# Performance work log

Measured on AMD Instinct MI355X. Metric: run time of the kernel, lower is better.

The kernel has to match this reference:

```python
import jax, jax.numpy as jnp
import numpy as np

G, NP, C, H, L = 64, 512, 128, 4, 4
N = G * NP            # 32768 nodes
E = N * 16            # 524288 edges
HD = C // H
BN_EPS = 1e-5


def _bn(x, g, b):
    # BatchNorm1d, training-mode (biased batch statistics over nodes)
    m = x.mean(axis=0)
    v = jnp.var(x, axis=0)
    return (x - m) * jax.lax.rsqrt(v + BN_EPS) * g + b


def setup_inputs() -> dict:
    key = jax.random.key(0)
    ks = iter(jax.random.split(key, 64))
    rn = lambda shape, s=0.05: jax.random.normal(next(ks), shape, jnp.float32) * s
    inp = {}
    inp["x"] = jax.random.normal(next(ks), (N, 32), jnp.float32)
    inp["edge_attr"] = jax.random.normal(next(ks), (E, 16), jnp.float32)
    epg = E // G  # edges per graph; endpoints stay within each graph
    off = jnp.repeat(jnp.arange(G), epg) * NP
    src = jax.random.randint(next(ks), (E,), 0, NP) + off
    dst = jax.random.randint(next(ks), (E,), 0, NP) + off
    inp["edge_index"] = jnp.stack([src, dst]).astype(jnp.int32)
    inp["batch"] = jnp.repeat(jnp.arange(G), NP).astype(jnp.int32)
    inp["np_w"] = rn((32, C)); inp["np_b"] = jnp.zeros((C,), jnp.float32)
    inp["ep_w"] = rn((16, C)); inp["ep_b"] = jnp.zeros((C,), jnp.float32)
    inp["eps"] = jnp.zeros((L,), jnp.float32)  # GINEConv train_eps, init 0
    inp["gine_w1"] = rn((L, C, 2 * C)); inp["gine_b1"] = jnp.zeros((L, 2 * C), jnp.float32)
    inp["gine_w2"] = rn((L, 2 * C, C)); inp["gine_b2"] = jnp.zeros((L, C), jnp.float32)
    inp["attn_in_w"] = rn((L, 3 * C, C)); inp["attn_in_b"] = jnp.zeros((L, 3 * C), jnp.float32)
    inp["attn_out_w"] = rn((L, C, C)); inp["attn_out_b"] = jnp.zeros((L, C), jnp.float32)
    ones = jnp.ones((L, C), jnp.float32); zeros = jnp.zeros((L, C), jnp.float32)
    inp["bn1_g"], inp["bn1_b"] = ones, zeros
    inp["bn2_g"], inp["bn2_b"] = ones, zeros
    inp["bn3_g"], inp["bn3_b"] = ones, zeros
    inp["mlp_w1"] = rn((L, C, 2 * C)); inp["mlp_b1"] = jnp.zeros((L, 2 * C), jnp.float32)
    inp["mlp_w2"] = rn((L, 2 * C, C)); inp["mlp_b2"] = jnp.zeros((L, C), jnp.float32)
    inp["ln_g"] = jnp.ones((2 * C,), jnp.float32); inp["ln_b"] = jnp.zeros((2 * C,), jnp.float32)
    inp["head_w1"] = rn((2 * C, C)); inp["head_b1"] = jnp.zeros((C,), jnp.float32)
    inp["head_w2"] = rn((C, 1)); inp["head_b2"] = jnp.zeros((1,), jnp.float32)
    return inp


def reference(x, edge_attr, np_w, np_b, ep_w, ep_b, eps,
              gine_w1, gine_b1, gine_w2, gine_b2,
              attn_in_w, attn_in_b, attn_out_w, attn_out_b,
              bn1_g, bn1_b, bn2_g, bn2_b, bn3_g, bn3_b,
              mlp_w1, mlp_b1, mlp_w2, mlp_b2,
              ln_g, ln_b, head_w1, head_b1, head_w2, head_b2,
              edge_index, batch):
    h = x @ np_w + np_b                       # [N, C]
    e = edge_attr @ ep_w + ep_b               # [E, C]
    src, dst = edge_index[0], edge_index[1]   # PyG: row=source j, col=target i
    scale = 1.0 / np.sqrt(HD).astype(np.float32)
    for l in range(L):
        # ---- local GINEConv: relu(x_j + e) scatter-sum -> GELU MLP ----
        msg = jax.nn.relu(h[src] + e)                                 # [E, C]
        aggr = jax.ops.segment_sum(msg, dst, num_segments=N)          # [N, C]
        z = (1.0 + eps[l]) * h + aggr
        z = jax.nn.gelu(z @ gine_w1[l] + gine_b1[l], approximate=False) @ gine_w2[l] + gine_b2[l]
        h_local = _bn(z + h, bn1_g[l], bn1_b[l])
        # ---- global multihead attention on dense per-graph batch ----
        xd = h.reshape(G, NP, C)
        qkv = xd @ attn_in_w[l].T + attn_in_b[l]                      # [G, NP, 3C]
        q, k, v = jnp.split(qkv, 3, axis=-1)
        split_heads = lambda t: t.reshape(G, NP, H, HD).transpose(0, 2, 1, 3)
        q, k, v = split_heads(q), split_heads(k), split_heads(v)
        att = jax.nn.softmax(jnp.einsum('ghqd,ghkd->ghqk', q, k) * scale, axis=-1)
        o = jnp.einsum('ghqk,ghkd->ghqd', att, v).transpose(0, 2, 1, 3).reshape(N, C)
        o = o @ attn_out_w[l].T + attn_out_b[l]
        h_attn = _bn(o + h, bn2_g[l], bn2_b[l])
        # ---- combine + FFN ----
        out = h_local + h_attn
        m = jax.nn.relu(out @ mlp_w1[l] + mlp_b1[l]) @ mlp_w2[l] + mlp_b2[l]
        h = _bn(out + m, bn3_g[l], bn3_b[l])
    # ---- mean || max pooling over graphs ----
    cnt = jax.ops.segment_sum(jnp.ones((N, 1), h.dtype), batch, num_segments=G)
    x_mean = jax.ops.segment_sum(h, batch, num_segments=G) / cnt
    x_max = jax.ops.segment_max(h, batch, num_segments=G)
    g = jnp.concatenate([x_mean, x_max], axis=-1)                     # [G, 2C]
    mu = g.mean(-1, keepdims=True)
    var = jnp.var(g, axis=-1, keepdims=True)
    g = (g - mu) * jax.lax.rsqrt(var + 1e-5) * ln_g + ln_b
    g = jax.nn.gelu(g @ head_w1 + head_b1, approximate=False) @ head_w2 + head_b2
    return g.squeeze(-1)                                              # [G]
```

## Files before the change

kernel.cpp:

```cpp
#include <hip/hip_runtime.h>
#include <math.h>

typedef _Float16 f16;
typedef _Float16 f16x2 __attribute__((ext_vector_type(2)));
typedef _Float16 f16x4 __attribute__((ext_vector_type(4)));
typedef _Float16 f16x8 __attribute__((ext_vector_type(8)));
typedef float f32x4 __attribute__((ext_vector_type(4)));

#define G_ 64
#define NP_ 512
#define N_ 32768
#define E_ 524288
#define C_ 128
#define H_ 4
#define HD_ 32
#define L_ 4

static __device__ __forceinline__ float gelu_exact(float x) {
    return 0.5f * x * (1.0f + erff(x * 0.70710678118654752f));
}

__global__ __launch_bounds__(256) void k_prep(
    const float* __restrict__ g1, const float* __restrict__ g2,
    const float* __restrict__ m1, const float* __restrict__ m2,
    const float* __restrict__ ai, const float* __restrict__ ao,
    f16* __restrict__ g1t, f16* __restrict__ g2t,
    f16* __restrict__ m1t, f16* __restrict__ m2t,
    f16* __restrict__ ait, f16* __restrict__ aot)
{
    int i = blockIdx.x * 256 + threadIdx.x;
    if (i < 131072) {
        int l = i >> 15, r = i & 32767;
        int k = r >> 8, m = r & 255;
        g1t[l * 32768 + m * 128 + k] = (f16)g1[i];
    } else if (i < 262144) {
        int j = i - 131072;
        int l = j >> 15, r = j & 32767;
        int k = r >> 7, m = r & 127;
        g2t[l * 32768 + m * 256 + k] = (f16)g2[j];
    } else if (i < 393216) {
        int j = i - 262144;
        int l = j >> 15, r = j & 32767;
        int k = r >> 8, m = r & 255;
        m1t[l * 32768 + m * 128 + k] = (f16)m1[j];
    } else if (i < 524288) {
        int j = i - 393216;
        int l = j >> 15, r = j & 32767;
        int k = r >> 7, m = r & 127;
        m2t[l * 32768 + m * 256 + k] = (f16)m2[j];
    } else if (i < 720896) {
        int j = i - 524288;
        ait[j] = (f16)ai[j];
    } else if (i < 786432) {
        int j = i - 720896;
        aot[j] = (f16)ao[j];
    }
}

__global__ __launch_bounds__(256) void k_h0(const float* __restrict__ x,
    const float* __restrict__ w, const float* __restrict__ b,
    f16* __restrict__ h16)
{
    const int tid = threadIdx.x;
    const int lane = tid & 63, wid = tid >> 6;
    const int node = blockIdx.x * 4 + wid;
    const int c2 = lane * 2;
    float a0 = b[c2], a1 = b[c2 + 1];
    const float* xr = x + (size_t)node * 32;
#pragma unroll
    for (int k = 0; k < 32; k++) {
        float xv = xr[k];
        a0 += xv * w[k * 128 + c2];
        a1 += xv * w[k * 128 + c2 + 1];
    }
    f16x2 z; z[0] = (f16)a0; z[1] = (f16)a1;
    *(f16x2*)(h16 + (size_t)node * 128 + c2) = z;
}

__global__ void k_zero2(int* a, int* b) {
    int i = blockIdx.x * 256 + threadIdx.x;
    a[i] = 0; b[i] = 0;
}
__global__ void k_count(const int* __restrict__ ei, int* __restrict__ counts) {
    int e = blockIdx.x * 256 + threadIdx.x;
    atomicAdd(&counts[ei[E_ + e]], 1);
}
__global__ __launch_bounds__(1024) void k_scan(const int* __restrict__ counts,
                                               int* __restrict__ rowp)
{
    __shared__ int part[1024];
    const int t = threadIdx.x;
    int s = 0;
#pragma unroll
    for (int i = 0; i < 32; i++) s += counts[t * 32 + i];
    part[t] = s;
    __syncthreads();
    for (int off = 1; off < 1024; off <<= 1) {
        int u = (t >= off) ? part[t - off] : 0;
        __syncthreads();
        part[t] += u;
        __syncthreads();
    }
    int run = part[t] - s;
    for (int i = 0; i < 32; i++) {
        int c = counts[t * 32 + i];
        rowp[t * 32 + i] = run;
        run += c;
    }
    if (t == 1023) rowp[N_] = part[1023];
}
__global__ void k_fill(const int* __restrict__ ei, const int* __restrict__ rowp,
                       int* __restrict__ cursor, int* __restrict__ srcp,
                       int* __restrict__ eidp)
{
    int e = blockIdx.x * 256 + threadIdx.x;
    int d = ei[E_ + e];
    int p = atomicAdd(&cursor[d], 1);
    int pos = rowp[d] + p;
    srcp[pos] = ei[e];
    eidp[pos] = e;
}

__global__ __launch_bounds__(256) void k_edge(const float* __restrict__ edge_attr,
    const float* __restrict__ epw, const float* __restrict__ epb,
    const int* __restrict__ eidp, f16* __restrict__ e16p)
{
    __shared__ __align__(16) float rows[4][64][16];
    const int tid = threadIdx.x;
    const int lane = tid & 63, wid = tid >> 6;
    const int c2 = lane * 2;
    float w0[16], w1[16];
#pragma unroll
    for (int k = 0; k < 16; k++) {
        w0[k] = epw[k * 128 + c2];
        w1[k] = epw[k * 128 + c2 + 1];
    }
    const float b0 = epb[c2], b1 = epb[c2 + 1];
    const int gidx = blockIdx.x & 63, chunk = blockIdx.x >> 6;
    const int base = (gidx * 32 + chunk) * 256 + wid * 64;
    const int eidv = eidp[base + lane];
    const int er = lane >> 2, ec = lane & 3;
#pragma unroll
    for (int u = 0; u < 4; u++) {
        int e = __shfl(eidv, u * 16 + er);
        float4 v = *(const float4*)(edge_attr + (size_t)e * 16 + ec * 4);
        *(float4*)(&rows[wid][u * 16 + er][ec * 4]) = v;
    }
    for (int i = 0; i < 64; i++) {
        const float* r = &rows[wid][i][0];
        float4 q0 = *(const float4*)(r);
        float4 q1 = *(const float4*)(r + 4);
        float4 q2 = *(const float4*)(r + 8);
        float4 q3 = *(const float4*)(r + 12);
        float e0 = b0, e1 = b1;
        e0 += q0.x*w0[0] + q0.y*w0[1] + q0.z*w0[2] + q0.w*w0[3]
            + q1.x*w0[4] + q1.y*w0[5] + q1.z*w0[6] + q1.w*w0[7]
            + q2.x*w0[8] + q2.y*w0[9] + q2.z*w0[10] + q2.w*w0[11]
            + q3.x*w0[12] + q3.y*w0[13] + q3.z*w0[14] + q3.w*w0[15];
        e1 += q0.x*w1[0] + q0.y*w1[1] + q0.z*w1[2] + q0.w*w1[3]
            + q1.x*w1[4] + q1.y*w1[5] + q1.z*w1[6] + q1.w*w1[7]
            + q2.x*w1[8] + q2.y*w1[9] + q2.z*w1[10] + q2.w*w1[11]
            + q3.x*w1[12] + q3.y*w1[13] + q3.z*w1[14] + q3.w*w1[15];
        f16x2 z; z[0] = (f16)e0; z[1] = (f16)e1;
        *(f16x2*)(e16p + (size_t)(base + i) * 128 + c2) = z;
    }
}

__global__ __launch_bounds__(256) void k_aggr(const f16* __restrict__ h16,
    const f16* __restrict__ e16p, const int* __restrict__ srcp,
    const int* __restrict__ rowp, const float* __restrict__ eps, int layer,
    f16* __restrict__ zin)
{
    const int tid = threadIdx.x;
    const int lane = tid & 63, wid = tid >> 6;
    const int node = (blockIdx.x & 63) * 512 + (blockIdx.x >> 6) * 4 + wid;
    const int c2 = lane * 2;
    const int r0 = rowp[node], r1 = rowp[node + 1];
    const int deg = r1 - r0;
    const f16x2 hn = *(const f16x2*)(h16 + (size_t)node * 128 + c2);
    float a0 = 0.f, a1 = 0.f;
    if (deg > 0) {
        const int dd = deg < 64 ? deg : 64;
        const int jm = dd - 1;
        const int srcv = srcp[r0 + (lane < jm ? lane : jm)];
        f16x2 h_c, e_c, h_n, e_n;
        {
            int s = __shfl(srcv, 0);
            h_c = *(const f16x2*)(h16 + (size_t)s * 128 + c2);
            e_c = *(const f16x2*)(e16p + (size_t)r0 * 128 + c2);
            int j1 = 1 < jm ? 1 : jm;
            int s1 = __shfl(srcv, j1);
            h_n = *(const f16x2*)(h16 + (size_t)s1 * 128 + c2);
            e_n = *(const f16x2*)(e16p + (size_t)(r0 + j1) * 128 + c2);
        }
        for (int j = 0; j < dd; ++j) {
            int j2 = j + 2 < jm ? j + 2 : jm;
            int s2 = __shfl(srcv, j2);
            f16x2 h_f = *(const f16x2*)(h16 + (size_t)s2 * 128 + c2);
            f16x2 e_f = *(const f16x2*)(e16p + (size_t)(r0 + j2) * 128 + c2);
            a0 += fmaxf((float)e_c[0] + (float)h_c[0], 0.0f);
            a1 += fmaxf((float)e_c[1] + (float)h_c[1], 0.0f);
            h_c = h_n; e_c = e_n; h_n = h_f; e_n = e_f;
        }
        for (int pos = r0 + 64; pos < r1; ++pos) {
            int s = srcp[pos];
            f16x2 ev = *(const f16x2*)(e16p + (size_t)pos * 128 + c2);
            f16x2 hv = *(const f16x2*)(h16 + (size_t)s * 128 + c2);
            a0 += fmaxf((float)ev[0] + (float)hv[0], 0.0f);
            a1 += fmaxf((float)ev[1] + (float)hv[1], 0.0f);
        }
    }
    const float ep = 1.0f + eps[layer];
    f16x2 z;
    z[0] = (f16)(ep * (float)hn[0] + a0);
    z[1] = (f16)(ep * (float)hn[1] + a1);
    *(f16x2*)(zin + (size_t)node * 128 + c2) = z;
}

template <int KD, int EPI, bool COMB>
__global__ __launch_bounds__(256) void k_gemm(
    const f16* __restrict__ A, const f16* __restrict__ Bt,
    const float* __restrict__ bias,
    const f16* __restrict__ r1, const f16* __restrict__ r2,
    const float* __restrict__ sc1, const float* __restrict__ sc2,
    f16* __restrict__ out, f16* __restrict__ aout,
    float* __restrict__ stats, int Mout)
{
    __shared__ __align__(16) f16 As[64 * 40];
    __shared__ __align__(16) f16 Bs[128 * 40];
    __shared__ float sca[4][128];
    __shared__ float sscr[4][2][64];
    const int tid = threadIdx.x;
    const int lane = tid & 63, wid = tid >> 6;
    const int quad = lane >> 4, l16 = lane & 15;
    const int wm = wid >> 1, wn = wid & 1;
    const int rb = blockIdx.x, cb = blockIdx.y;
    if constexpr (COMB) {
        if (tid < 128) { sca[0][tid] = sc1[tid]; sca[1][tid] = sc1[128 + tid]; }
        else { int c = tid - 128; sca[2][c] = sc2[c]; sca[3][c] = sc2[128 + c]; }
    }
    f32x4 acc[2][4];
#pragma unroll
    for (int i = 0; i < 2; i++)
#pragma unroll
        for (int j = 0; j < 4; j++) acc[i][j] = {0.f, 0.f, 0.f, 0.f};
    const int arow0 = rb * 64, brow0 = cb * 128;
    const int srow = tid >> 2, sc4 = tid & 3;
#pragma unroll
    for (int kc = 0; kc < KD / 32; ++kc) {
        __syncthreads();
        if constexpr (COMB) {
            size_t off = (size_t)(arow0 + srow) * KD + kc * 32 + sc4 * 8;
            f16x8 x1 = *(const f16x8*)(r1 + off);
            f16x8 x2 = *(const f16x8*)(r2 + off);
            const int k0 = kc * 32 + sc4 * 8;
            f16x8 zc;
#pragma unroll
            for (int i = 0; i < 8; i++) {
                int k = k0 + i;
                float v = (float)x1[i] * sca[0][k] + sca[1][k]
                        + (float)x2[i] * sca[2][k] + sca[3][k];
                zc[i] = (f16)v;
            }
            *(f16x8*)(As + srow * 40 + sc4 * 8) = zc;
            if (cb == 0) *(f16x8*)(aout + off) = zc;
        } else {
            *(uint4*)(As + srow * 40 + sc4 * 8) =
                *(const uint4*)(A + (size_t)(arow0 + srow) * KD + kc * 32 + sc4 * 8);
        }
#pragma unroll
        for (int i = 0; i < 2; i++) {
            int j = tid + i * 256;
            int br = j >> 2, bc = j & 3;
            *(uint4*)(Bs + br * 40 + bc * 8) =
                *(const uint4*)(Bt + (size_t)(brow0 + br) * KD + kc * 32 + bc * 8);
        }
        __syncthreads();
        f16x8 af[2], bf[4];
#pragma unroll
        for (int mt = 0; mt < 2; mt++)
            af[mt] = *(const f16x8*)(As + (wm * 32 + mt * 16 + l16) * 40 + quad * 8);
#pragma unroll
        for (int nt = 0; nt < 4; nt++)
            bf[nt] = *(const f16x8*)(Bs + (wn * 64 + nt * 16 + l16) * 40 + quad * 8);
#pragma unroll
        for (int mt = 0; mt < 2; mt++)
#pragma unroll
            for (int nt = 0; nt < 4; nt++)
                acc[mt][nt] = __builtin_amdgcn_mfma_f32_16x16x32_f16(
                    af[mt], bf[nt], acc[mt][nt], 0, 0, 0);
    }
    float ssum[4] = {0, 0, 0, 0}, ssq[4] = {0, 0, 0, 0};
#pragma unroll
    for (int nt = 0; nt < 4; nt++) {
        const int col = cb * 128 + wn * 64 + nt * 16 + l16;
        const float bv = bias[col];
#pragma unroll
        for (int mt = 0; mt < 2; mt++) {
#pragma unroll
            for (int r = 0; r < 4; r++) {
                const int row = rb * 64 + wm * 32 + mt * 16 + quad * 4 + r;
                float v = acc[mt][nt][r] + bv;
                if constexpr (EPI == 0) v = gelu_exact(v);
                if constexpr (EPI == 1) v = fmaxf(v, 0.0f);
                if constexpr (EPI == 2) {
                    v += (float)r1[(size_t)row * 128 + col];
                    ssum[nt] += v;
                    ssq[nt] += v * v;
                }
                out[(size_t)row * Mout + col] = (f16)v;
            }
        }
    }
    if constexpr (EPI == 2) {
#pragma unroll
        for (int nt = 0; nt < 4; nt++) {
            float s = ssum[nt], q = ssq[nt];
            s += __shfl_xor(s, 16); s += __shfl_xor(s, 32);
            q += __shfl_xor(q, 16); q += __shfl_xor(q, 32);
            if (lane < 16) {
                sscr[wid][0][nt * 16 + lane] = s;
                sscr[wid][1][nt * 16 + lane] = q;
            }
        }
        __syncthreads();
        if (tid < 128) {
            int c = tid, wnc = c >> 6, jj = c & 63;
            stats[(size_t)rb * 256 + c] = sscr[wnc][0][jj] + sscr[wnc + 2][0][jj];
            stats[(size_t)rb * 256 + 128 + c] = sscr[wnc][1][jj] + sscr[wnc + 2][1][jj];
        }
    }
}

__global__ __launch_bounds__(256) void k_qkv(
    const f16* __restrict__ A, const f16* __restrict__ Bt,
    const float* __restrict__ bias,
    f16* __restrict__ qb, f16* __restrict__ kb, f16* __restrict__ vt)
{
    __shared__ __align__(16) f16 As[64 * 40];
    __shared__ __align__(16) f16 Bs[128 * 40];
    const int tid = threadIdx.x;
    const int lane = tid & 63, wid = tid >> 6;
    const int quad = lane >> 4, l16 = lane & 15;
    const int wm = wid >> 1, wn = wid & 1;
    const int rb = blockIdx.x, cb = blockIdx.y;
    f32x4 acc[2][4];
#pragma unroll
    for (int i = 0; i < 2; i++)
#pragma unroll
        for (int j = 0; j < 4; j++) acc[i][j] = {0.f, 0.f, 0.f, 0.f};
    const int arow0 = rb * 64, brow0 = cb * 128;
    const int srow = tid >> 2, sc4 = tid & 3;
#pragma unroll
    for (int kc = 0; kc < 4; ++kc) {
        __syncthreads();
        *(uint4*)(As + srow * 40 + sc4 * 8) =
            *(const uint4*)(A + (size_t)(arow0 + srow) * 128 + kc * 32 + sc4 * 8);
#pragma unroll
        for (int i = 0; i < 2; i++) {
            int j = tid + i * 256;
            int br = j >> 2, bc = j & 3;
            *(uint4*)(Bs + br * 40 + bc * 8) =
                *(const uint4*)(Bt + (size_t)(brow0 + br) * 128 + kc * 32 + bc * 8);
        }
        __syncthreads();
        f16x8 af[2], bf[4];
#pragma unroll
        for (int mt = 0; mt < 2; mt++)
            af[mt] = *(const f16x8*)(As + (wm * 32 + mt * 16 + l16) * 40 + quad * 8);
#pragma unroll
        for (int nt = 0; nt < 4; nt++)
            bf[nt] = *(const f16x8*)(Bs + (wn * 64 + nt * 16 + l16) * 40 + quad * 8);
#pragma unroll
        for (int mt = 0; mt < 2; mt++)
#pragma unroll
            for (int nt = 0; nt < 4; nt++)
                acc[mt][nt] = __builtin_amdgcn_mfma_f32_16x16x32_f16(
                    af[mt], bf[nt], acc[mt][nt], 0, 0, 0);
    }
    if (cb < 2) {
        f16* outp = cb ? kb : qb;
#pragma unroll
        for (int nt = 0; nt < 4; nt++) {
            const int col = wn * 64 + nt * 16 + l16;
            const float bv = bias[cb * 128 + col];
#pragma unroll
            for (int mt = 0; mt < 2; mt++) {
#pragma unroll
                for (int r = 0; r < 4; r++) {
                    const int row = rb * 64 + wm * 32 + mt * 16 + quad * 4 + r;
                    outp[(size_t)row * 128 + col] = (f16)(acc[mt][nt][r] + bv);
                }
            }
        }
    } else {
        const int g = rb >> 3;
#pragma unroll
        for (int nt = 0; nt < 4; nt++) {
            const int coll = wn * 64 + nt * 16 + l16;
            const int h = coll >> 5, d = coll & 31;
            const float bv = bias[256 + coll];
#pragma unroll
            for (int mt = 0; mt < 2; mt++) {
                const int n0 = (rb & 7) * 64 + wm * 32 + mt * 16 + quad * 4;
                f16x4 z;
#pragma unroll
                for (int r = 0; r < 4; r++) z[r] = (f16)(acc[mt][nt][r] + bv);
                *(f16x4*)(vt + ((size_t)((g * 4 + h) * 32 + d)) * 512 + n0) = z;
            }
        }
    }
}

__global__ __launch_bounds__(1024) void k_fin(
    const float* __restrict__ sA, const float* __restrict__ sB,
    const float* __restrict__ g1, const float* __restrict__ b1,
    const float* __restrict__ g2, const float* __restrict__ b2,
    float* __restrict__ o1, float* __restrict__ o2)
{
    __shared__ float rS[8][128], rQ[8][128];
    const float* s = blockIdx.x ? sB : sA;
    const float* g = blockIdx.x ? g2 : g1;
    const float* bb = blockIdx.x ? b2 : b1;
    float* o = blockIdx.x ? o2 : o1;
    const int c = threadIdx.x & 127, seg = threadIdx.x >> 7;
    float S = 0, Q = 0;
    for (int b = seg * 64; b < seg * 64 + 64; b++) {
        S += s[b * 256 + c];
        Q += s[b * 256 + 128 + c];
    }
    rS[seg][c] = S; rQ[seg][c] = Q;
    __syncthreads();
    if (threadIdx.x < 128) {
        float Ss = 0, Qs = 0;
#pragma unroll
        for (int k = 0; k < 8; k++) { Ss += rS[k][c]; Qs += rQ[k][c]; }
        float mean = Ss * (1.0f / 32768.0f);
        float var = Qs * (1.0f / 32768.0f) - mean * mean;
        float rstd = rsqrtf(var + 1e-5f);
        float scv = g[c] * rstd;
        o[c] = scv;
        o[128 + c] = bb[c] - mean * scv;
    }
}

__global__ __launch_bounds__(256) void k_bn3(const f16* __restrict__ t3,
    const float* __restrict__ s3, f16* __restrict__ h16)
{
    int i = blockIdx.x * 256 + threadIdx.x;
    int n = i >> 6, c2 = (i & 63) * 2;
    f16x2 a = *(const f16x2*)(t3 + (size_t)n * 128 + c2);
    f16x2 z;
    z[0] = (f16)((float)a[0] * s3[c2] + s3[128 + c2]);
    z[1] = (f16)((float)a[1] * s3[c2 + 1] + s3[129 + c2]);
    *(f16x2*)(h16 + (size_t)n * 128 + c2) = z;
}

__global__ __launch_bounds__(256) void k_attn(const f16* __restrict__ qb,
    const f16* __restrict__ kb, const f16* __restrict__ vt, f16* __restrict__ o)
{
    __shared__ __align__(16) f16 Ks[512 * 36];
    __shared__ __align__(16) f16 Ps[4][512];
    const int tid = threadIdx.x;
    const int lane = tid & 63, wid = tid >> 6;
    const int quad = lane >> 4, l16 = lane & 15;
    const int blk = blockIdx.x;
    const int gh = blk & 255, qc = blk >> 8;
    const int g = gh >> 2, h = gh & 3;
#pragma unroll
    for (int i = 0; i < 8; i++) {
        int j = i * 256 + tid;
        int n = j >> 2, c4 = j & 3;
        *(uint4*)(Ks + n * 36 + c4 * 8) =
            *(const uint4*)(kb + (size_t)(g * 512 + n) * 128 + h * 32 + c4 * 8);
    }
    const int node = g * 512 + qc * 64 + wid * 16 + l16;
    f16x8 aq = *(const f16x8*)(qb + (size_t)node * 128 + h * 32 + quad * 8);
    __syncthreads();
    const f32x4 zero = {0.f, 0.f, 0.f, 0.f};
    const float cexp = 0.17677669529663689f * 1.44269504088896341f;
    float m = -1e30f;
    for (int kt = 0; kt < 32; ++kt) {
        f16x8 ak = *(const f16x8*)(Ks + (kt * 16 + l16) * 36 + quad * 8);
        f32x4 s = __builtin_amdgcn_mfma_f32_16x16x32_f16(ak, aq, zero, 0, 0, 0);
        m = fmaxf(m, fmaxf(fmaxf(s[0], s[1]), fmaxf(s[2], s[3])));
    }
    m = fmaxf(m, __shfl_xor(m, 16));
    m = fmaxf(m, __shfl_xor(m, 32));
    float lsum = 0.f;
    f32x4 o0 = {0.f, 0.f, 0.f, 0.f}, o1 = {0.f, 0.f, 0.f, 0.f};
    f16* pp = &Ps[wid][0];
    const f16* vbase = vt + (size_t)gh * 32 * 512;
    const int roff = quad * 128;
    for (int ch = 0; ch < 16; ++ch) {
        f16x8 ak0 = *(const f16x8*)(Ks + ((2 * ch) * 16 + l16) * 36 + quad * 8);
        f16x8 ak1 = *(const f16x8*)(Ks + ((2 * ch + 1) * 16 + l16) * 36 + quad * 8);
        f32x4 s0 = __builtin_amdgcn_mfma_f32_16x16x32_f16(ak0, aq, zero, 0, 0, 0);
        f32x4 s1 = __builtin_amdgcn_mfma_f32_16x16x32_f16(ak1, aq, zero, 0, 0, 0);
        f16x4 p0, p1;
#pragma unroll
        for (int r = 0; r < 4; r++) {
            float e0 = exp2f((s0[r] - m) * cexp);
            float e1 = exp2f((s1[r] - m) * cexp);
            lsum += e0 + e1;
            p0[r] = (f16)e0; p1[r] = (f16)e1;
        }
        *(f16x4*)(pp + lane * 4) = p0;
        *(f16x4*)(pp + 256 + lane * 4) = p1;
        f16x4 a_lo = *(const f16x4*)(pp + roff + l16 * 4);
        f16x4 a_hi = *(const f16x4*)(pp + roff + 64 + l16 * 4);
        f16x8 ap;
#pragma unroll
        for (int i2 = 0; i2 < 4; i2++) { ap[i2] = a_lo[i2]; ap[i2 + 4] = a_hi[i2]; }
        f16x8 bv0 = *(const f16x8*)(vbase + (size_t)l16 * 512 + ch * 32 + quad * 8);
        f16x8 bv1 = *(const f16x8*)(vbase + (size_t)(16 + l16) * 512 + ch * 32 + quad * 8);
        o0 = __builtin_amdgcn_mfma_f32_16x16x32_f16(ap, bv0, o0, 0, 0, 0);
        o1 = __builtin_amdgcn_mfma_f32_16x16x32_f16(ap, bv1, o1, 0, 0, 0);
    }
    lsum += __shfl_xor(lsum, 16);
    lsum += __shfl_xor(lsum, 32);
    const float linv = 1.0f / lsum;
#pragma unroll
    for (int r = 0; r < 4; r++) {
        float li = __shfl(linv, quad * 4 + r);
        int nrow = g * 512 + qc * 64 + wid * 16 + quad * 4 + r;
        o[(size_t)nrow * 128 + h * 32 + l16] = (f16)(o0[r] * li);
        o[(size_t)nrow * 128 + h * 32 + 16 + l16] = (f16)(o1[r] * li);
    }
}

__global__ __launch_bounds__(256) void k_pool(const f16* __restrict__ h16,
    const float* __restrict__ ln_g, const float* __restrict__ ln_b,
    const float* __restrict__ w1, const float* __restrict__ b1,
    const float* __restrict__ w2, const float* __restrict__ b2,
    float* __restrict__ outp)
{
    __shared__ float ssum[4][128], smax[4][128];
    __shared__ float gl[256];
    __shared__ float red[256];
    __shared__ float hid[128];
    __shared__ float stat[2];
    const int tid = threadIdx.x, lane = tid & 63, wid = tid >> 6;
    const int g = blockIdx.x;
    const int c2 = lane * 2;
    float s0 = 0, s1 = 0, m0 = -1e30f, m1 = -1e30f;
    for (int i = 0; i < 128; i++) {
        int n = g * 512 + i * 4 + wid;
        f16x2 hv = *(const f16x2*)(h16 + (size_t)n * 128 + c2);
        float v0 = (float)hv[0], v1 = (float)hv[1];
        s0 += v0; s1 += v1;
        m0 = fmaxf(m0, v0); m1 = fmaxf(m1, v1);
    }
    ssum[wid][c2] = s0; ssum[wid][c2 + 1] = s1;
    smax[wid][c2] = m0; smax[wid][c2 + 1] = m1;
    __syncthreads();
    if (tid < 128) {
        float S = ssum[0][tid] + ssum[1][tid] + ssum[2][tid] + ssum[3][tid];
        float M = fmaxf(fmaxf(smax[0][tid], smax[1][tid]),
                        fmaxf(smax[2][tid], smax[3][tid]));
        gl[tid] = S * (1.0f / 512.0f);
        gl[128 + tid] = M;
    }
    __syncthreads();
    float v = gl[tid];
    red[tid] = v;
    __syncthreads();
    for (int off = 128; off > 0; off >>= 1) {
        if (tid < off) red[tid] += red[tid + off];
        __syncthreads();
    }
    if (tid == 0) stat[0] = red[0] * (1.0f / 256.0f);
    __syncthreads();
    float mu = stat[0];
    red[tid] = (v - mu) * (v - mu);
    __syncthreads();
    for (int off = 128; off > 0; off >>= 1) {
        if (tid < off) red[tid] += red[tid + off];
        __syncthreads();
    }
    if (tid == 0) stat[1] = rsqrtf(red[0] * (1.0f / 256.0f) + 1e-5f);
    __syncthreads();
    float gn = (v - mu) * stat[1] * ln_g[tid] + ln_b[tid];
    __syncthreads();
    gl[tid] = gn;
    __syncthreads();
    if (tid < 128) {
        float a = b1[tid];
        for (int k = 0; k < 256; k++) a += gl[k] * w1[k * 128 + tid];
        hid[tid] = gelu_exact(a);
    }
    __syncthreads();
    if (tid < 64) {
        float a = hid[tid] * w2[tid] + hid[tid + 64] * w2[tid + 64];
        a += __shfl_xor(a, 32); a += __shfl_xor(a, 16); a += __shfl_xor(a, 8);
        a += __shfl_xor(a, 4); a += __shfl_xor(a, 2); a += __shfl_xor(a, 1);
        if (tid == 0) outp[g] = a + b2[0];
    }
}

extern "C" void kernel_launch(void* const* d_in, const int* in_sizes, int n_in,
                              void* d_out, int out_size, void* d_ws, size_t ws_size,
                              hipStream_t stream)
{
    const float* x          = (const float*)d_in[0];
    const float* edge_attr  = (const float*)d_in[1];
    const int*   ei         = (const int*)d_in[2];
    const float* np_w       = (const float*)d_in[4];
    const float* np_b       = (const float*)d_in[5];
    const float* ep_w       = (const float*)d_in[6];
    const float* ep_b       = (const float*)d_in[7];
    const float* eps        = (const float*)d_in[8];
    const float* gine_w1    = (const float*)d_in[9];
    const float* gine_b1    = (const float*)d_in[10];
    const float* gine_w2    = (const float*)d_in[11];
    const float* gine_b2    = (const float*)d_in[12];
    const float* attn_in_w  = (const float*)d_in[13];
    const float* attn_in_b  = (const float*)d_in[14];
    const float* attn_out_w = (const float*)d_in[15];
    const float* attn_out_b = (const float*)d_in[16];
    const float* bn1_g      = (const float*)d_in[17];
    const float* bn1_b      = (const float*)d_in[18];
    const float* bn2_g      = (const float*)d_in[19];
    const float* bn2_b      = (const float*)d_in[20];
    const float* bn3_g      = (const float*)d_in[21];
    const float* bn3_b      = (const float*)d_in[22];
    const float* mlp_w1     = (const float*)d_in[23];
    const float* mlp_b1     = (const float*)d_in[24];
    const float* mlp_w2     = (const float*)d_in[25];
    const float* mlp_b2     = (const float*)d_in[26];
    const float* ln_g       = (const float*)d_in[27];
    const float* ln_b       = (const float*)d_in[28];
    const float* head_w1    = (const float*)d_in[29];
    const float* head_b1    = (const float*)d_in[30];
    const float* head_w2    = (const float*)d_in[31];
    const float* head_b2    = (const float*)d_in[32];

    char* ws = (char*)d_ws;
    size_t off = 0;
    auto alloc = [&](size_t bytes) {
        void* p = ws + off;
        off += (bytes + 255) & ~(size_t)255;
        return p;
    };
    f16*  h16    = (f16*)alloc((size_t)N_ * 128 * 2);
    f16*  zin    = (f16*)alloc((size_t)N_ * 128 * 2);
    f16*  tloc   = (f16*)alloc((size_t)N_ * 128 * 2);
    f16*  tattn  = (f16*)alloc((size_t)N_ * 128 * 2);
    f16*  out16  = (f16*)alloc((size_t)N_ * 128 * 2);
    f16*  o16    = (f16*)alloc((size_t)N_ * 128 * 2);
    f16*  u16    = (f16*)alloc((size_t)N_ * 256 * 2);
    float* statsA = (float*)alloc(512 * 256 * 4);
    float* statsB = (float*)alloc(512 * 256 * 4);
    float* scsh1  = (float*)alloc(256 * 4);
    float* scsh2  = (float*)alloc(256 * 4);
    float* scsh3  = (float*)alloc(256 * 4);
    int*  rowp   = (int*)alloc((N_ + 1) * 4);
    int*  counts = (int*)alloc(N_ * 4);
    int*  cursor = (int*)alloc(N_ * 4);
    int*  srcp   = (int*)alloc((size_t)E_ * 4);
    int*  eidp   = (int*)alloc((size_t)E_ * 4);
    f16*  g1t    = (f16*)alloc((size_t)L_ * 32768 * 2);
    f16*  g2t    = (f16*)alloc((size_t)L_ * 32768 * 2);
    f16*  m1t    = (f16*)alloc((size_t)L_ * 32768 * 2);
    f16*  m2t    = (f16*)alloc((size_t)L_ * 32768 * 2);
    f16*  ait    = (f16*)alloc((size_t)L_ * 49152 * 2);
    f16*  aot    = (f16*)alloc((size_t)L_ * 16384 * 2);
    f16*  e16p   = (f16*)alloc((size_t)E_ * 128 * 2);
    f16*  qbuf = zin;
    f16*  kbuf = out16;
    f16*  vt   = u16 + (size_t)N_ * 128;

    dim3 B(256);
    k_prep<<<dim3(3072), B, 0, stream>>>(gine_w1, gine_w2, mlp_w1, mlp_w2,
                                         attn_in_w, attn_out_w,
                                         g1t, g2t, m1t, m2t, ait, aot);
    k_h0<<<dim3(8192), B, 0, stream>>>(x, np_w, np_b, h16);
    k_zero2<<<dim3(128), B, 0, stream>>>(counts, cursor);
    k_count<<<dim3(2048), B, 0, stream>>>(ei, counts);
    k_scan<<<dim3(1), dim3(1024), 0, stream>>>(counts, rowp);
    k_fill<<<dim3(2048), B, 0, stream>>>(ei, rowp, cursor, srcp, eidp);
    k_edge<<<dim3(2048), B, 0, stream>>>(edge_attr, ep_w, ep_b, eidp, e16p);

    const f16* nf = (const f16*)nullptr;
    const float* nff = (const float*)nullptr;
    for (int l = 0; l < L_; l++) {
        k_aggr<<<dim3(8192), B, 0, stream>>>(h16, e16p, srcp, rowp, eps, l, zin);
        k_gemm<128, 0, false><<<dim3(512, 2), B, 0, stream>>>(
            zin, g1t + l * 32768, gine_b1 + l * 256, nf, nf, nff, nff,
            u16, (f16*)nullptr, (float*)nullptr, 256);
        k_gemm<256, 2, false><<<dim3(512, 1), B, 0, stream>>>(
            u16, g2t + l * 32768, gine_b2 + l * 128, h16, nf, nff, nff,
            tloc, (f16*)nullptr, statsA, 128);
        k_qkv<<<dim3(512, 3), B, 0, stream>>>(
            h16, ait + l * 49152, attn_in_b + l * 384, qbuf, kbuf, vt);
        k_attn<<<dim3(2048), B, 0, stream>>>(qbuf, kbuf, vt, o16);
        k_gemm<128, 2, false><<<dim3(512, 1), B, 0, stream>>>(
            o16, aot + l * 16384, attn_out_b + l * 128, h16, nf, nff, nff,
            tattn, (f16*)nullptr, statsB, 128);
        k_fin<<<dim3(2), dim3(1024), 0, stream>>>(
            statsA, statsB, bn1_g + l * 128, bn1_b + l * 128,
            bn2_g + l * 128, bn2_b + l * 128, scsh1, scsh2);
        k_gemm<128, 1, true><<<dim3(512, 2), B, 0, stream>>>(
            nf, m1t + l * 32768, mlp_b1 + l * 256, tloc, tattn, scsh1, scsh2,
            u16, out16, (float*)nullptr, 256);
        k_gemm<256, 2, false><<<dim3(512, 1), B, 0, stream>>>(
            u16, m2t + l * 32768, mlp_b2 + l * 128, out16, nf, nff, nff,
            zin, (f16*)nullptr, statsA, 128);
        k_fin<<<dim3(1), dim3(1024), 0, stream>>>(
            statsA, statsA, bn3_g + l * 128, bn3_b + l * 128,
            bn3_g + l * 128, bn3_b + l * 128, scsh3, scsh3);
        k_bn3<<<dim3(8192), B, 0, stream>>>(zin, scsh3, h16);
    }
    k_pool<<<dim3(64), B, 0, stream>>>(h16, ln_g, ln_b, head_w1, head_b1,
                                       head_w2, head_b2, (float*)d_out);
}
```

Before: 978.8 us.

## Load GEMM tiles via global_load_lds with XOR swizzle and merge output GEMMs

GEMM kernels now stage the full 128-wide K slab into LDS with direct global-to-LDS loads, using an XOR-swizzled layout instead of padded rows. This removes the per-32-K-chunk barriers and register round trips. The GINE second GEMM and the attention output projection are merged into one launch, k_g2, which splits work by blockIdx.y. The v-transpose buffer is moved to tloc to avoid aliasing u16. In exchange the kernels use more LDS per block, which may lower occupancy, and k_g2 now has a runtime K loop.

```diff
diff --git a/kernel.cpp b/kernel.cpp
--- a/kernel.cpp
+++ b/kernel.cpp
@@ -18,6 +18,12 @@
 
 static __device__ __forceinline__ float gelu_exact(float x) {
     return 0.5f * x * (1.0f + erff(x * 0.70710678118654752f));
+}
+
+static __device__ __forceinline__ void gload_lds(const f16* g, f16* l) {
+    __builtin_amdgcn_global_load_lds(
+        (const __attribute__((address_space(1))) void*)g,
+        (__attribute__((address_space(3))) void*)l, 16, 0, 0);
 }
 
 __global__ __launch_bounds__(256) void k_prep(
@@ -217,72 +223,84 @@
     *(f16x2*)(zin + (size_t)node * 128 + c2) = z;
 }
 
-template <int KD, int EPI, bool COMB>
-__global__ __launch_bounds__(256) void k_gemm(
+
+template <int EPI, bool COMB>
+__global__ __launch_bounds__(256) void k_g128(
     const f16* __restrict__ A, const f16* __restrict__ Bt,
     const float* __restrict__ bias,
     const f16* __restrict__ r1, const f16* __restrict__ r2,
     const float* __restrict__ sc1, const float* __restrict__ sc2,
-    f16* __restrict__ out, f16* __restrict__ aout,
-    float* __restrict__ stats, int Mout)
-{
-    __shared__ __align__(16) f16 As[64 * 40];
-    __shared__ __align__(16) f16 Bs[128 * 40];
+    f16* __restrict__ out, f16* __restrict__ aout, int Mout)
+{
+    __shared__ __align__(16) f16 Sm[3072 * 8];
     __shared__ float sca[4][128];
-    __shared__ float sscr[4][2][64];
+    f16* As = Sm;
+    f16* Bs = Sm + 1024 * 8;
     const int tid = threadIdx.x;
     const int lane = tid & 63, wid = tid >> 6;
     const int quad = lane >> 4, l16 = lane & 15;
     const int wm = wid >> 1, wn = wid & 1;
     const int rb = blockIdx.x, cb = blockIdx.y;
-    if constexpr (COMB) {
+    const int arow0 = rb * 64, brow0 = cb * 128;
+#pragma unroll
+    for (int i = 0; i < 8; i++) {
+        int s = i * 256 + wid * 64 + lane;
+        int r = s >> 4, cg = (s & 15) ^ (r & 7);
+        gload_lds(Bt + (size_t)(brow0 + r) * 128 + cg * 8,
+                  Bs + (size_t)(i * 256 + wid * 64) * 8);
+    }
+    if constexpr (!COMB) {
+#pragma unroll
+        for (int i = 0; i < 4; i++) {
+            int s = i * 256 + wid * 64 + lane;
+            int r = s >> 4, cg = (s & 15) ^ (r & 7);
+            gload_lds(A + (size_t)(arow0 + r) * 128 + cg * 8,
+                      As + (size_t)(i * 256 + wid * 64) * 8);
+        }
+        __syncthreads();
+    } else {
         if (tid < 128) { sca[0][tid] = sc1[tid]; sca[1][tid] = sc1[128 + tid]; }
         else { int c = tid - 128; sca[2][c] = sc2[c]; sca[3][c] = sc2[128 + c]; }
-    }
-    f32x4 acc[2][4];
-#pragma unroll
-    for (int i = 0; i < 2; i++)
-#pragma unroll
-        for (int j = 0; j < 4; j++) acc[i][j] = {0.f, 0.f, 0.f, 0.f};
-    const int arow0 = rb * 64, brow0 = cb * 128;
-    const int srow = tid >> 2, sc4 = tid & 3;
-#pragma unroll
-    for (int kc = 0; kc < KD / 32; ++kc) {
         __syncthreads();
-        if constexpr (COMB) {
-            size_t off = (size_t)(arow0 + srow) * KD + kc * 32 + sc4 * 8;
+#pragma unroll
+        for (int j = 0; j < 4; j++) {
+            int s = j * 256 + tid;
+            int r = s >> 4, cg = (s & 15) ^ (r & 7);
+            size_t off = (size_t)(arow0 + r) * 128 + cg * 8;
             f16x8 x1 = *(const f16x8*)(r1 + off);
             f16x8 x2 = *(const f16x8*)(r2 + off);
-            const int k0 = kc * 32 + sc4 * 8;
             f16x8 zc;
 #pragma unroll
-            for (int i = 0; i < 8; i++) {
-                int k = k0 + i;
-                float v = (float)x1[i] * sca[0][k] + sca[1][k]
-                        + (float)x2[i] * sca[2][k] + sca[3][k];
-                zc[i] = (f16)v;
+            for (int i2 = 0; i2 < 8; i2++) {
+                int k = cg * 8 + i2;
+                float v = (float)x1[i2] * sca[0][k] + sca[1][k]
+                        + (float)x2[i2] * sca[2][k] + sca[3][k];
+                zc[i2] = (f16)v;
             }
-            *(f16x8*)(As + srow * 40 + sc4 * 8) = zc;
+            *(f16x8*)(As + (size_t)s * 8) = zc;
             if (cb == 0) *(f16x8*)(aout + off) = zc;
-        } else {
-            *(uint4*)(As + srow * 40 + sc4 * 8) =
-                *(const uint4*)(A + (size_t)(arow0 + srow) * KD + kc * 32 + sc4 * 8);
-        }
-#pragma unroll
-        for (int i = 0; i < 2; i++) {
-            int j = tid + i * 256;
-            int br = j >> 2, bc = j & 3;
-            *(uint4*)(Bs + br * 40 + bc * 8) =
-                *(const uint4*)(Bt + (size_t)(brow0 + br) * KD + kc * 32 + bc * 8);
         }
         __syncthreads();
+    }
+    f32x4 acc[2][4];
+#pragma unroll
+    for (int i = 0; i < 2; i++)
+#pragma unroll
+        for (int j = 0; j < 4; j++) acc[i][j] = {0.f, 0.f, 0.f, 0.f};
+    const int ra0 = wm * 32 + l16, rb0 = wn * 64 + l16;
+#pragma unroll
+    for (int kc = 0; kc < 4; ++kc) {
         f16x8 af[2], bf[4];
 #pragma unroll
-        for (int mt = 0; mt < 2; mt++)
-            af[mt] = *(const f16x8*)(As + (wm * 32 + mt * 16 + l16) * 40 + quad * 8);
-#pragma unroll
-        for (int nt = 0; nt < 4; nt++)
-            bf[nt] = *(const f16x8*)(Bs + (wn * 64 + nt * 16 + l16) * 40 + quad * 8);
+        for (int mt = 0; mt < 2; mt++) {
+            int r = ra0 + mt * 16;
+            af[mt] = *(const f16x8*)(As + (size_t)(r * 16 + ((kc * 4 + quad) ^ (r & 7))) * 8);
+        }
+#pragma unroll
+        for (int nt = 0; nt < 4; nt++) {
+            int r = rb0 + nt * 16;
+            bf[nt] = *(const f16x8*)(Bs + (size_t)(r * 16 + ((kc * 4 + quad) ^ (r & 7))) * 8);
+        }
 #pragma unroll
         for (int mt = 0; mt < 2; mt++)
 #pragma unroll
@@ -290,7 +308,6 @@
                 acc[mt][nt] = __builtin_amdgcn_mfma_f32_16x16x32_f16(
                     af[mt], bf[nt], acc[mt][nt], 0, 0, 0);
     }
-    float ssum[4] = {0, 0, 0, 0}, ssq[4] = {0, 0, 0, 0};
 #pragma unroll
     for (int nt = 0; nt < 4; nt++) {
         const int col = cb * 128 + wn * 64 + nt * 16 + l16;
@@ -303,74 +320,166 @@
                 float v = acc[mt][nt][r] + bv;
                 if constexpr (EPI == 0) v = gelu_exact(v);
                 if constexpr (EPI == 1) v = fmaxf(v, 0.0f);
-                if constexpr (EPI == 2) {
-                    v += (float)r1[(size_t)row * 128 + col];
-                    ssum[nt] += v;
-                    ssq[nt] += v * v;
-                }
                 out[(size_t)row * Mout + col] = (f16)v;
             }
         }
     }
-    if constexpr (EPI == 2) {
-#pragma unroll
-        for (int nt = 0; nt < 4; nt++) {
-            float s = ssum[nt], q = ssq[nt];
-            s += __shfl_xor(s, 16); s += __shfl_xor(s, 32);
-            q += __shfl_xor(q, 16); q += __shfl_xor(q, 32);
-            if (lane < 16) {
-                sscr[wid][0][nt * 16 + lane] = s;
-                sscr[wid][1][nt * 16 + lane] = q;
-            }
-        }
-        __syncthreads();
-        if (tid < 128) {
-            int c = tid, wnc = c >> 6, jj = c & 63;
-            stats[(size_t)rb * 256 + c] = sscr[wnc][0][jj] + sscr[wnc + 2][0][jj];
-            stats[(size_t)rb * 256 + 128 + c] = sscr[wnc][1][jj] + sscr[wnc + 2][1][jj];
-        }
-    }
-}
-
-__global__ __launch_bounds__(256) void k_qkv(
-    const f16* __restrict__ A, const f16* __restrict__ Bt,
-    const float* __restrict__ bias,
-    f16* __restrict__ qb, f16* __restrict__ kb, f16* __restrict__ vt)
-{
-    __shared__ __align__(16) f16 As[64 * 40];
-    __shared__ __align__(16) f16 Bs[128 * 40];
+}
+
+__global__ __launch_bounds__(256) void k_g2(
+    const f16* __restrict__ A0, const f16* __restrict__ Bt0,
+    const float* __restrict__ bias0,
+    const f16* __restrict__ A1, const f16* __restrict__ Bt1,
+    const float* __restrict__ bias1,
+    const f16* __restrict__ resid,
+    f16* __restrict__ out0, f16* __restrict__ out1,
+    float* __restrict__ stats0, float* __restrict__ stats1)
+{
+    __shared__ __align__(16) f16 Sm[3072 * 8];
+    __shared__ float sscr[4][2][64];
+    f16* As = Sm;
+    f16* Bs = Sm + 1024 * 8;
     const int tid = threadIdx.x;
     const int lane = tid & 63, wid = tid >> 6;
     const int quad = lane >> 4, l16 = lane & 15;
     const int wm = wid >> 1, wn = wid & 1;
     const int rb = blockIdx.x, cb = blockIdx.y;
+    const int arow0 = rb * 64;
+    const f16* A  = cb ? A1 : A0;
+    const f16* Bt = cb ? Bt1 : Bt0;
+    const float* bias = cb ? bias1 : bias0;
+    f16* out = cb ? out1 : out0;
+    float* stats = cb ? stats1 : stats0;
+    const int KD = cb ? 128 : 256;
+    const int npass = KD >> 7;
     f32x4 acc[2][4];
 #pragma unroll
     for (int i = 0; i < 2; i++)
 #pragma unroll
         for (int j = 0; j < 4; j++) acc[i][j] = {0.f, 0.f, 0.f, 0.f};
+    const int ra0 = wm * 32 + l16, rb0 = wn * 64 + l16;
+    for (int p = 0; p < npass; ++p) {
+        if (p) __syncthreads();
+#pragma unroll
+        for (int i = 0; i < 4; i++) {
+            int s = i * 256 + wid * 64 + lane;
+            int r = s >> 4, cg = (s & 15) ^ (r & 7);
+            gload_lds(A + (size_t)(arow0 + r) * KD + p * 128 + cg * 8,
+                      As + (size_t)(i * 256 + wid * 64) * 8);
+        }
+#pragma unroll
+        for (int i = 0; i < 8; i++) {
+            int s = i * 256 + wid * 64 + lane;
+            int r = s >> 4, cg = (s & 15) ^ (r & 7);
+            gload_lds(Bt + (size_t)r * KD + p * 128 + cg * 8,
+                      Bs + (size_t)(i * 256 + wid * 64) * 8);
+        }
+        __syncthreads();
+#pragma unroll
+        for (int kc = 0; kc < 4; ++kc) {
+            f16x8 af[2], bf[4];
+#pragma unroll
+            for (int mt = 0; mt < 2; mt++) {
+                int r = ra0 + mt * 16;
+                af[mt] = *(const f16x8*)(As + (size_t)(r * 16 + ((kc * 4 + quad) ^ (r & 7))) * 8);
+            }
+#pragma unroll
+            for (int nt = 0; nt < 4; nt++) {
+                int r = rb0 + nt * 16;
+                bf[nt] = *(const f16x8*)(Bs + (size_t)(r * 16 + ((kc * 4 + quad) ^ (r & 7))) * 8);
+            }
+#pragma unroll
+            for (int mt = 0; mt < 2; mt++)
+#pragma unroll
+                for (int nt = 0; nt < 4; nt++)
+                    acc[mt][nt] = __builtin_amdgcn_mfma_f32_16x16x32_f16(
+                        af[mt], bf[nt], acc[mt][nt], 0, 0, 0);
+        }
+    }
+    float ssum[4] = {0, 0, 0, 0}, ssq[4] = {0, 0, 0, 0};
+#pragma unroll
+    for (int nt = 0; nt < 4; nt++) {
+        const int col = wn * 64 + nt * 16 + l16;
+        const float bv = bias[col];
+#pragma unroll
+        for (int mt = 0; mt < 2; mt++) {
+#pragma unroll
+            for (int r = 0; r < 4; r++) {
+                const int row = rb * 64 + wm * 32 + mt * 16 + quad * 4 + r;
+                float v = acc[mt][nt][r] + bv;
+                v += (float)resid[(size_t)row * 128 + col];
+                ssum[nt] += v;
+                ssq[nt] += v * v;
+                out[(size_t)row * 128 + col] = (f16)v;
+            }
+        }
+    }
+#pragma unroll
+    for (int nt = 0; nt < 4; nt++) {
+        float s = ssum[nt], q = ssq[nt];
+        s += __shfl_xor(s, 16); s += __shfl_xor(s, 32);
+        q += __shfl_xor(q, 16); q += __shfl_xor(q, 32);
+        if (lane < 16) {
+            sscr[wid][0][nt * 16 + lane] = s;
+            sscr[wid][1][nt * 16 + lane] = q;
+        }
+    }
+    __syncthreads();
+    if (tid < 128) {
+        int c = tid, wnc = c >> 6, jj = c & 63;
+        stats[(size_t)rb * 256 + c] = sscr[wnc][0][jj] + sscr[wnc + 2][0][jj];
+        stats[(size_t)rb * 256 + 128 + c] = sscr[wnc][1][jj] + sscr[wnc + 2][1][jj];
+    }
+}
+
+__global__ __launch_bounds__(256) void k_qkv(
+    const f16* __restrict__ A, const f16* __restrict__ Bt,
+    const float* __restrict__ bias,
+    f16* __restrict__ qb, f16* __restrict__ kb, f16* __restrict__ vt)
+{
+    __shared__ __align__(16) f16 Sm[3072 * 8];
+    f16* As = Sm;
+    f16* Bs = Sm + 1024 * 8;
+    const int tid = threadIdx.x;
+    const int lane = tid & 63, wid = tid >> 6;
+    const int quad = lane >> 4, l16 = lane & 15;
+    const int wm = wid >> 1, wn = wid & 1;
+    const int rb = blockIdx.x, cb = blockIdx.y;
     const int arow0 = rb * 64, brow0 = cb * 128;
-    const int srow = tid >> 2, sc4 = tid & 3;
+#pragma unroll
+    for (int i = 0; i < 8; i++) {
+        int s = i * 256 + wid * 64 + lane;
+        int r = s >> 4, cg = (s & 15) ^ (r & 7);
+        gload_lds(Bt + (size_t)(brow0 + r) * 128 + cg * 8,
+                  Bs + (size_t)(i * 256 + wid * 64) * 8);
+    }
+#pragma unroll
+    for (int i = 0; i < 4; i++) {
+        int s = i * 256 + wid * 64 + lane;
+        int r = s >> 4, cg = (s & 15) ^ (r & 7);
+        gload_lds(A + (size_t)(arow0 + r) * 128 + cg * 8,
+                  As + (size_t)(i * 256 + wid * 64) * 8);
+    }
+    __syncthreads();
+    f32x4 acc[2][4];
+#pragma unroll
+    for (int i = 0; i < 2; i++)
+#pragma unroll
+        for (int j = 0; j < 4; j++) acc[i][j] = {0.f, 0.f, 0.f, 0.f};
+    const int ra0 = wm * 32 + l16, rb0 = wn * 64 + l16;
 #pragma unroll
     for (int kc = 0; kc < 4; ++kc) {
-        __syncthreads();
-        *(uint4*)(As + srow * 40 + sc4 * 8) =
-            *(const uint4*)(A + (size_t)(arow0 + srow) * 128 + kc * 32 + sc4 * 8);
-#pragma unroll
-        for (int i = 0; i < 2; i++) {
-            int j = tid + i * 256;
-            int br = j >> 2, bc = j & 3;
-            *(uint4*)(Bs + br * 40 + bc * 8) =
-                *(const uint4*)(Bt + (size_t)(brow0 + br) * 128 + kc * 32 + bc * 8);
-        }
-        __syncthreads();
         f16x8 af[2], bf[4];
 #pragma unroll
-        for (int mt = 0; mt < 2; mt++)
-            af[mt] = *(const f16x8*)(As + (wm * 32 + mt * 16 + l16) * 40 + quad * 8);
-#pragma unroll
-        for (int nt = 0; nt < 4; nt++)
-            bf[nt] = *(const f16x8*)(Bs + (wn * 64 + nt * 16 + l16) * 40 + quad * 8);
+        for (int mt = 0; mt < 2; mt++) {
+            int r = ra0 + mt * 16;
+            af[mt] = *(const f16x8*)(As + (size_t)(r * 16 + ((kc * 4 + quad) ^ (r & 7))) * 8);
+        }
+#pragma unroll
+        for (int nt = 0; nt < 4; nt++) {
+            int r = rb0 + nt * 16;
+            bf[nt] = *(const f16x8*)(Bs + (size_t)(r * 16 + ((kc * 4 + quad) ^ (r & 7))) * 8);
+        }
 #pragma unroll
         for (int mt = 0; mt < 2; mt++)
 #pragma unroll
@@ -668,7 +777,7 @@
     f16*  e16p   = (f16*)alloc((size_t)E_ * 128 * 2);
     f16*  qbuf = zin;
     f16*  kbuf = out16;
-    f16*  vt   = u16 + (size_t)N_ * 128;
+    f16*  vt   = tloc;
 
     dim3 B(256);
     k_prep<<<dim3(3072), B, 0, stream>>>(gine_w1, gine_w2, mlp_w1, mlp_w2,
@@ -685,27 +794,26 @@
     const float* nff = (const float*)nullptr;
     for (int l = 0; l < L_; l++) {
         k_aggr<<<dim3(8192), B, 0, stream>>>(h16, e16p, srcp, rowp, eps, l, zin);
-        k_gemm<128, 0, false><<<dim3(512, 2), B, 0, stream>>>(
+        k_g128<0, false><<<dim3(512, 2), B, 0, stream>>>(
             zin, g1t + l * 32768, gine_b1 + l * 256, nf, nf, nff, nff,
-            u16, (f16*)nullptr, (float*)nullptr, 256);
-        k_gemm<256, 2, false><<<dim3(512, 1), B, 0, stream>>>(
-            u16, g2t + l * 32768, gine_b2 + l * 128, h16, nf, nff, nff,
-            tloc, (f16*)nullptr, statsA, 128);
+            u16, (f16*)nullptr, 256);
         k_qkv<<<dim3(512, 3), B, 0, stream>>>(
             h16, ait + l * 49152, attn_in_b + l * 384, qbuf, kbuf, vt);
         k_attn<<<dim3(2048), B, 0, stream>>>(qbuf, kbuf, vt, o16);
-        k_gemm<128, 2, false><<<dim3(512, 1), B, 0, stream>>>(
-            o16, aot + l * 16384, attn_out_b + l * 128, h16, nf, nff, nff,
-            tattn, (f16*)nullptr, statsB, 128);
+        k_g2<<<dim3(512, 2), B, 0, stream>>>(
+            u16, g2t + l * 32768, gine_b2 + l * 128,
+            o16, aot + l * 16384, attn_out_b + l * 128,
+            h16, tloc, tattn, statsA, statsB);
         k_fin<<<dim3(2), dim3(1024), 0, stream>>>(
             statsA, statsB, bn1_g + l * 128, bn1_b + l * 128,
             bn2_g + l * 128, bn2_b + l * 128, scsh1, scsh2);
-        k_gemm<128, 1, true><<<dim3(512, 2), B, 0, stream>>>(
+        k_g128<1, true><<<dim3(512, 2), B, 0, stream>>>(
             nf, m1t + l * 32768, mlp_b1 + l * 256, tloc, tattn, scsh1, scsh2,
-            u16, out16, (float*)nullptr, 256);
-        k_gemm<256, 2, false><<<dim3(512, 1), B, 0, stream>>>(
-            u16, m2t + l * 32768, mlp_b2 + l * 128, out16, nf, nff, nff,
-            zin, (f16*)nullptr, statsA, 128);
+            u16, out16, 256);
+        k_g2<<<dim3(512, 1), B, 0, stream>>>(
+            u16, m2t + l * 32768, mlp_b2 + l * 128,
+            u16, m2t + l * 32768, mlp_b2 + l * 128,
+            out16, zin, zin, statsA, statsA);
         k_fin<<<dim3(1), dim3(1024), 0, stream>>>(
             statsA, statsA, bn3_g + l * 128, bn3_b + l * 128,
             bn3_g + l * 128, bn3_b + l * 128, scsh3, scsh3);
```

After: 956.2 us. 1.02x faster.
